# Kernel optimization log

Measured on AMD Instinct MI355X. Metric: run time of the kernel, lower is better.

## Reference

```python
import jax, jax.numpy as jnp
import numpy as np

B, T, C, H = 4, 2048, 2048, 16
D = C // H  # head dim = 128


def setup_inputs() -> dict:
    key = jax.random.key(0)
    k1, k2, k3, k4 = jax.random.split(key, 4)
    x = jax.random.normal(k1, (B, T, C), dtype=jnp.float32)
    # per-token key mask; force token 0 valid so no causal row is fully masked
    tok_mask = jax.random.randint(k2, (B, T), 0, 2).astype(bool).at[:, 0].set(True)
    s = 1.0 / np.sqrt(C).astype(np.float32)
    W_qkv = jax.random.normal(k3, (C, 3 * C), dtype=jnp.float32) * s
    W_proj = jax.random.normal(k4, (C, C), dtype=jnp.float32) * s
    return {"x": x, "tok_mask": tok_mask, "W_qkv": W_qkv, "W_proj": W_proj}


def reference(x, tok_mask, W_qkv, W_proj):
    Bx, Tx, Cx = x.shape
    qkv = x @ W_qkv                              # [B,T,3C]
    q, k, v = jnp.split(qkv, 3, axis=-1)
    q = q.reshape(Bx, Tx, H, D)
    k = k.reshape(Bx, Tx, H, D)
    v = v.reshape(Bx, Tx, H, D)
    scale = 1.0 / np.sqrt(D).astype(np.float32)
    scores = jnp.einsum('bqhd,bkhd->bhqk', q, k) * scale  # [B,H,T,T]
    causal = jnp.tril(jnp.ones((Tx, Tx), dtype=bool))      # [T,T]
    # tok_mask broadcasts over the query dim (key mask), AND-ed with causal
    mask = tok_mask[:, None, :] & causal                   # [B,T,T]
    scores = jnp.where(mask[:, None, :, :], scores, -jnp.inf)
    attn = jax.nn.softmax(scores, axis=-1)                 # dropout p=0 -> identity
    y = jnp.einsum('bhqk,bkhd->bqhd', attn, v).reshape(Bx, Tx, Cx)
    return y @ W_proj
```

## Files before the change

### kernel.cpp

```cpp
#include <hip/hip_runtime.h>
#include <hip/hip_bf16.h>
#include <stdint.h>

typedef __bf16 bf16;
typedef __bf16 bf16x8 __attribute__((ext_vector_type(8)));
typedef float f32x4 __attribute__((ext_vector_type(4)));
typedef unsigned short u16;
typedef unsigned int u32;

constexpr int NB = 4;
constexpr int NT = 2048;
constexpr int NC = 2048;
constexpr int NH = 16;
constexpr int ND = 128;
constexpr int NC3 = 6144;

__device__ __forceinline__ void gload16(const void* g, void* l) {
  __builtin_amdgcn_global_load_lds((const __attribute__((address_space(1))) void*)g,
                                   (__attribute__((address_space(3))) void*)l, 16, 0, 0);
}

__device__ __forceinline__ u32 pack_bf16(float a, float b) {
  return (u32)__builtin_bit_cast(u16, (bf16)a) | ((u32)__builtin_bit_cast(u16, (bf16)b) << 16);
}

__global__ __launch_bounds__(256) void ingest_k(const float* __restrict__ raw, bf16* __restrict__ out, long n) {
  long i = ((long)blockIdx.x * 256 + threadIdx.x) * 8;
  if (i >= n) return;
  f32x4 a = *(const f32x4*)(raw + i), b = *(const f32x4*)(raw + i + 4);
  bf16x8 o;
  o[0] = (bf16)a[0]; o[1] = (bf16)a[1]; o[2] = (bf16)a[2]; o[3] = (bf16)a[3];
  o[4] = (bf16)b[0]; o[5] = (bf16)b[1]; o[6] = (bf16)b[2]; o[7] = (bf16)b[3];
  *(bf16x8*)(out + i) = o;
}

__global__ void mask_prep_k(const void* raw, char* out) {
  __shared__ int s_gt1, s_oddnz, s_allb, s_allf, s_allh;
  if (threadIdx.x == 0) { s_gt1 = 0; s_oddnz = 0; s_allb = 1; s_allf = 1; s_allh = 1; }
  __syncthreads();
  const unsigned int* mw = (const unsigned int*)raw;
  int gt1 = 0, oddnz = 0, allb = 1, allf = 1, allh = 1;
  for (int i = threadIdx.x; i < 2048; i += 256) {
    unsigned v = mw[i];
    if (v > 1u) gt1 = 1;
    if ((i & 1) && v) oddnz = 1;
#pragma unroll
    for (int bb = 0; bb < 4; ++bb) { unsigned by = (v >> (8*bb)) & 0xffu; if (by > 1u) allb = 0; }
    if (v != 0u && v != 0x3F800000u) allf = 0;
    unsigned lo = v & 0xffffu, hi = v >> 16;
    if ((lo != 0u && lo != 0x3F80u) || (hi != 0u && hi != 0x3F80u)) allh = 0;
  }
  if (gt1) atomicOr(&s_gt1, 1);
  if (oddnz) atomicOr(&s_oddnz, 1);
  if (!allb) atomicAnd(&s_allb, 0);
  if (!allf) atomicAnd(&s_allf, 0);
  if (!allh) atomicAnd(&s_allh, 0);
  __syncthreads();
  int mode;
  if (!s_gt1)       mode = s_oddnz ? 0 : 2;
  else if (s_allf)  mode = 3;
  else if (s_allb)  mode = 1;
  else if (s_allh)  mode = 4;
  else              mode = 0;
  for (int i = threadIdx.x; i < NB*NT; i += 256) {
    int v;
    if (mode == 0)      v = (((const int*)raw)[i] != 0);
    else if (mode == 1) v = (((const unsigned char*)raw)[i] != 0);
    else if (mode == 2) v = (((const long long*)raw)[i] != 0);
    else if (mode == 3) v = (((const unsigned int*)raw)[i] != 0);
    else                v = (((const unsigned short*)raw)[i] != 0);
    out[i] = (char)v;
  }
}

__global__ __launch_bounds__(256) void transpose_f32_k(const float* __restrict__ in, bf16* __restrict__ out,
                                                       int in_rs, int out_rs) {
  __shared__ __align__(16) bf16 t[64][72];
  const int r0 = blockIdx.y << 6, c0 = blockIdx.x << 6;
  const int tid = threadIdx.x;
#pragma unroll
  for (int i = 0; i < 4; ++i) {
    int slot = i*256 + tid, row = slot >> 4, c4 = slot & 15;
    f32x4 v = *(const f32x4*)(in + (long)(r0 + row)*in_rs + c0 + c4*4);
#pragma unroll
    for (int e = 0; e < 4; ++e) t[c4*4 + e][row] = (bf16)v[e];
  }
  __syncthreads();
#pragma unroll
  for (int i = 0; i < 2; ++i) {
    int slot = i*256 + tid, row = slot >> 3, c8 = slot & 7;
    bf16x8 v = *(const bf16x8*)(&t[row][c8*8]);
    *(bf16x8*)(out + (long)(c0 + row)*out_rs + r0 + c8*8) = v;
  }
}

__global__ __launch_bounds__(256) void vtrans_k(const bf16* __restrict__ qkv, bf16* __restrict__ vt) {
  __shared__ __align__(16) bf16 t[64][72];
  const int tt = blockIdx.x, dh = blockIdx.y, bh = blockIdx.z;
  const int b = bh >> 4, h = bh & 15;
  const int tid = threadIdx.x;
  const bf16* src = qkv + (long)(b*NT + tt*64)*NC3 + (2*NC + h*ND + dh*64);
#pragma unroll
  for (int i = 0; i < 2; ++i) {
    int slot = i*256 + tid, row = slot >> 3, c8 = slot & 7;
    bf16x8 v = *(const bf16x8*)(src + (long)row*NC3 + c8*8);
#pragma unroll
    for (int e = 0; e < 8; ++e) t[c8*8 + e][row] = v[e];
  }
  __syncthreads();
  bf16* dst = vt + ((long)bh*ND + dh*64)*NT + tt*64;
#pragma unroll
  for (int i = 0; i < 2; ++i) {
    int slot = i*256 + tid, row = slot >> 3, c8 = slot & 7;
    bf16x8 v = *(const bf16x8*)(&t[row][c8*8]);
    *(bf16x8*)(dst + (long)row*NT + c8*8) = v;
  }
}

#define G256_READ_A(qm_) \
  _Pragma("unroll") \
  for (int mi = 0; mi < 4; ++mi) { \
    _Pragma("unroll") \
    for (int kk = 0; kk < 2; ++kk) { \
      const int ri = (qm_)*64 + mi*16 + r; \
      af[mi*2+kk] = *(const bf16x8*)(Ac + wm*16384 + ri*128 + (((kk*4 + g) ^ (ri & 7)) << 4)); \
    } \
  }
#define G256_READ_B(qn_) \
  _Pragma("unroll") \
  for (int ni = 0; ni < 2; ++ni) { \
    _Pragma("unroll") \
    for (int kk = 0; kk < 2; ++kk) { \
      const int ri = (qn_)*32 + ni*16 + r; \
      bfr[ni*2+kk] = *(const bf16x8*)(Bc + wn*8192 + ri*128 + (((kk*4 + g) ^ (ri & 7)) << 4)); \
    } \
  }
#define G256_MFMA(mb_, nb_) \
  __builtin_amdgcn_s_setprio(1); \
  _Pragma("unroll") \
  for (int mi = 0; mi < 4; ++mi) \
    _Pragma("unroll") \
    for (int ni = 0; ni < 2; ++ni) \
      _Pragma("unroll") \
      for (int kk = 0; kk < 2; ++kk) \
        acc[(mb_)+mi][(nb_)+ni] = __builtin_amdgcn_mfma_f32_16x16x32_bf16(af[mi*2+kk], bfr[ni*2+kk], acc[(mb_)+mi][(nb_)+ni], 0, 0, 0); \
  __builtin_amdgcn_s_setprio(0);
#define G256_EDGE(vm_) \
  asm volatile("s_waitcnt vmcnt(" #vm_ ")" ::: "memory"); \
  __builtin_amdgcn_s_barrier(); \
  __builtin_amdgcn_sched_barrier(0);
#define G256_EDGE_NOVM() \
  asm volatile("" ::: "memory"); \
  __builtin_amdgcn_s_barrier(); \
  __builtin_amdgcn_sched_barrier(0);

template <typename OT>
__global__ __launch_bounds__(512, 2) void gemm256_k(const bf16* __restrict__ A, const bf16* __restrict__ BT,
                                                    OT* __restrict__ Cout, int M, int N, int K, int nbx) {
  const int nwg = gridDim.x;
  const int bid = blockIdx.x;
  const int cpx = nwg >> 3;
  const int swz = (bid & 7) * cpx + (bid >> 3);
  const int bx = swz % nbx, by = swz / nbx;
  const long m0 = (long)by << 8, n0 = (long)bx << 8;

  const int tid = threadIdx.x, w = tid >> 6, l = tid & 63, g = l >> 4, r = l & 15;
  const int wm = w >> 2, wn = w & 3;

  __shared__ __align__(16) char As[2][32768];
  __shared__ __align__(16) char Bs[2][32768];

  long aoff2[4], boff2[4];
  int alds[4], blds[4];
#pragma unroll
  for (int i = 0; i < 4; ++i) {
    int s = i*256 + (tid & 255);
    int ri = s >> 3, c = s & 7, cp = c ^ (ri & 7);
    aoff2[i] = (m0 + wm*128 + ri) * (long)K + cp*8;
    alds[i] = wm*16384 + ((i*256 + (w & 3)*64) << 4);
    int s2 = i*128 + wm*64 + l;
    int ri2 = s2 >> 3, c2 = s2 & 7, cp2 = c2 ^ (ri2 & 7);
    boff2[i] = (n0 + wn*64 + ri2) * (long)K + cp2*8;
    blds[i] = wn*8192 + ((i*128 + wm*64) << 4);
  }

  const f32x4 z4 = {0.f, 0.f, 0.f, 0.f};
  f32x4 acc[8][4];
#pragma unroll
  for (int i = 0; i < 8; ++i)
#pragma unroll
    for (int j = 0; j < 4; ++j) acc[i][j] = z4;

  const int nk = K >> 6;
  gload16(A + aoff2[0], As[0] + alds[0]);
  gload16(A + aoff2[1], As[0] + alds[1]);
  gload16(BT + boff2[0], Bs[0] + blds[0]);
  gload16(BT + boff2[1], Bs[0] + blds[1]);
  gload16(A + aoff2[2], As[0] + alds[2]);
  gload16(A + aoff2[3], As[0] + alds[3]);
  gload16(BT + boff2[2], Bs[0] + blds[2]);
  gload16(BT + boff2[3], Bs[0] + blds[3]);
  G256_EDGE(4);

  bf16x8 af[8], bfr[4];

  for (int t = 0; t < nk - 1; ++t) {
    const int cur = t & 1;
    const char* Ac = As[cur];
    const char* Bc = Bs[cur];
    char* An = As[cur ^ 1];
    char* Bn = Bs[cur ^ 1];
    const long ko = (long)(t + 1) << 6;

    G256_READ_A(0); G256_READ_B(0);
    gload16(A + aoff2[0] + ko, An + alds[0]);
    gload16(A + aoff2[1] + ko, An + alds[1]);
    gload16(BT + boff2[0] + ko, Bn + blds[0]);
    gload16(BT + boff2[1] + ko, Bn + blds[1]);
    G256_MFMA(0, 0);
    G256_EDGE(6);

    G256_READ_A(1);
    gload16(A + aoff2[2] + ko, An + alds[2]);
    gload16(A + aoff2[3] + ko, An + alds[3]);
    gload16(BT + boff2[2] + ko, Bn + blds[2]);
    gload16(BT + boff2[3] + ko, Bn + blds[3]);
    G256_MFMA(4, 0);
    G256_EDGE(8);

    G256_READ_B(1);
    G256_MFMA(4, 2);
    G256_EDGE_NOVM();

    G256_READ_A(0);
    G256_MFMA(0, 2);
    G256_EDGE(4);
  }

  {
    const int cur = (nk - 1) & 1;
    const char* Ac = As[cur];
    const char* Bc = Bs[cur];
    G256_READ_A(0); G256_READ_B(0);
    G256_MFMA(0, 0);
    G256_EDGE(2);
    G256_READ_A(1);
    G256_MFMA(4, 0);
    G256_EDGE(0);
    G256_READ_B(1);
    G256_MFMA(4, 2);
    G256_EDGE_NOVM();
    G256_READ_A(0);
    G256_MFMA(0, 2);
  }

#pragma unroll
  for (int mi = 0; mi < 8; ++mi)
#pragma unroll
    for (int ni = 0; ni < 4; ++ni)
#pragma unroll
      for (int j = 0; j < 4; ++j) {
        long mr = m0 + wm*128 + mi*16 + 4*g + j;
        long nc = n0 + wn*64 + ni*16 + r;
        Cout[mr*(long)N + nc] = (OT)acc[mi][ni][j];
      }
}

__global__ __launch_bounds__(256, 2) void attn_k(const bf16* __restrict__ qkv, const bf16* __restrict__ vt,
                                                 const char* __restrict__ maskC, bf16* __restrict__ y) {
  const int qx = blockIdx.x, h = blockIdx.y, b = blockIdx.z;
  const int qb = (qx & 1) ? (15 - (qx >> 1)) : (qx >> 1);
  const int tid = threadIdx.x, w = tid >> 6, l = tid & 63, g = l >> 4, r = l & 15;
  const int q0 = qb << 7;
  const int bh = b*NH + h;
  const int ntiles = (qb << 1) + 2;
  const int qrowA = q0 + w*32 + r;
  const int qrowB = qrowA + 16;

  __shared__ __align__(16) char Klds[2][16384];
  __shared__ __align__(16) char Vlds[2][16384];
  __shared__ __align__(16) char Plds[16384];
  char* PlA = Plds + (w << 12);
  char* PlB = PlA + 2048;

  const char* mc = maskC + b*NT;

  long koff[4], voff[4];
  int klo[4];
#pragma unroll
  for (int i = 0; i < 4; ++i) {
    int slot = i*256 + tid;
    int row = slot >> 4, c = slot & 15, cp = c ^ (row & 7);
    koff[i] = (long)row*NC3 + cp*8;
    klo[i] = (i*256 + w*64) << 4;
    int vrow = slot >> 3, vc = slot & 7, vcp = vc ^ (vrow & 7);
    voff[i] = (long)vrow*NT + vcp*8;
  }
  const bf16* kbase0 = qkv + (long)(b*NT)*NC3 + (NC + h*ND);
  const bf16* vbase0 = vt + (long)bh*ND*NT;

  bf16x8 qfA[4], qfB[4];
  {
    const bf16* qpA = qkv + (long)(b*NT + qrowA)*NC3 + h*ND + g*8;
    const bf16* qpB = qkv + (long)(b*NT + qrowB)*NC3 + h*ND + g*8;
#pragma unroll
    for (int dk = 0; dk < 4; ++dk) {
      qfA[dk] = *(const bf16x8*)(qpA + dk*32);
      qfB[dk] = *(const bf16x8*)(qpB + dk*32);
    }
  }

  const f32x4 z4 = {0.f, 0.f, 0.f, 0.f};
  f32x4 accA[8], accB[8];
#pragma unroll
  for (int i = 0; i < 8; ++i) { accA[i] = z4; accB[i] = z4; }
  float m_runA = 0.0f, l_runA = 0.0f;
  float m_runB = 0.0f, l_runB = 0.0f;

  const float SCL = 0.08838834764831845f * 1.4426950408889634f;

#pragma unroll
  for (int i = 0; i < 4; ++i) {
    gload16(kbase0 + koff[i], Klds[0] + klo[i]);
    gload16(vbase0 + voff[i], Vlds[0] + klo[i]);
  }
  __syncthreads();

  for (int kt = 0; kt < ntiles; ++kt) {
    const int cur = kt & 1;
    if (kt + 1 < ntiles) {
      const bf16* kb = kbase0 + (long)((kt+1)*64)*NC3;
      const bf16* vb = vbase0 + (kt+1)*64;
#pragma unroll
      for (int i = 0; i < 4; ++i) {
        gload16(kb + koff[i], Klds[cur^1] + klo[i]);
        gload16(vb + voff[i], Vlds[cur^1] + klo[i]);
      }
    }
    const char* Kl = Klds[cur];
    const char* Vl = Vlds[cur];
    const int key0 = kt*64;
    const bool actB = (key0 <= q0 + w*32 + 31);
    const bool actA = (key0 <= q0 + w*32 + 15);

    if (actB) {
      u32 mw_[4];
#pragma unroll
      for (int kc = 0; kc < 4; ++kc) mw_[kc] = *(const u32*)(mc + key0 + kc*16 + 4*g);

      float tvA[4][4], tvB[4][4];
      __builtin_amdgcn_s_setprio(1);
#pragma unroll
      for (int kc = 0; kc < 4; ++kc) {
        const int krow = kc*16 + r;
        bf16x8 kf[4];
#pragma unroll
        for (int dk = 0; dk < 4; ++dk)
          kf[dk] = *(const bf16x8*)(Kl + krow*256 + (((dk*4 + g) ^ (krow & 7)) << 4));
        f32x4 sB = z4;
#pragma unroll
        for (int dk = 0; dk < 4; ++dk)
          sB = __builtin_amdgcn_mfma_f32_16x16x32_bf16(kf[dk], qfB[dk], sB, 0, 0, 0);
        f32x4 sA = z4;
        if (actA) {
#pragma unroll
          for (int dk = 0; dk < 4; ++dk)
            sA = __builtin_amdgcn_mfma_f32_16x16x32_bf16(kf[dk], qfA[dk], sA, 0, 0, 0);
        }
#pragma unroll
        for (int j = 0; j < 4; ++j) {
          const int key = key0 + kc*16 + 4*g + j;
          const bool km = ((mw_[kc] >> (8*j)) & 0xffu) != 0;
          tvB[kc][j] = (km && key <= qrowB) ? sB[j]*SCL : -3.0e38f;
          tvA[kc][j] = (km && key <= qrowA) ? sA[j]*SCL : -3.0e38f;
        }
      }
      __builtin_amdgcn_s_setprio(0);

      {
        float tmax = -3.0e38f;
#pragma unroll
        for (int kc = 0; kc < 4; ++kc)
#pragma unroll
          for (int j = 0; j < 4; ++j) tmax = fmaxf(tmax, tvB[kc][j]);
        tmax = fmaxf(tmax, __shfl_xor(tmax, 16));
        tmax = fmaxf(tmax, __shfl_xor(tmax, 32));
        if (!__all(tmax <= m_runB + 8.0f)) {
          float mn = fmaxf(m_runB, tmax);
          float al = exp2f(m_runB - mn);
          m_runB = mn;
          l_runB *= al;
          float alj[4];
#pragma unroll
          for (int j = 0; j < 4; ++j) alj[j] = __shfl(al, 4*g + j);
#pragma unroll
          for (int d0 = 0; d0 < 8; ++d0)
#pragma unroll
            for (int j = 0; j < 4; ++j) accB[d0][j] *= alj[j];
        }
        float rs = 0.f;
#pragma unroll
        for (int kc = 0; kc < 4; ++kc) {
          float p0 = exp2f(tvB[kc][0] - m_runB), p1 = exp2f(tvB[kc][1] - m_runB);
          float p2 = exp2f(tvB[kc][2] - m_runB), p3 = exp2f(tvB[kc][3] - m_runB);
          rs += (p0 + p1) + (p2 + p3);
          const int off = (kc*32 + g*8) ^ ((r & 7) << 4);
          uint2 wv; wv.x = pack_bf16(p0, p1); wv.y = pack_bf16(p2, p3);
          *(uint2*)(PlB + r*128 + off) = wv;
        }
        rs += __shfl_xor(rs, 16);
        rs += __shfl_xor(rs, 32);
        l_runB += rs;
      }
      if (actA) {
        float tmax = -3.0e38f;
#pragma unroll
        for (int kc = 0; kc < 4; ++kc)
#pragma unroll
          for (int j = 0; j < 4; ++j) tmax = fmaxf(tmax, tvA[kc][j]);
        tmax = fmaxf(tmax, __shfl_xor(tmax, 16));
        tmax = fmaxf(tmax, __shfl_xor(tmax, 32));
        if (!__all(tmax <= m_runA + 8.0f)) {
          float mn = fmaxf(m_runA, tmax);
          float al = exp2f(m_runA - mn);
          m_runA = mn;
          l_runA *= al;
          float alj[4];
#pragma unroll
          for (int j = 0; j < 4; ++j) alj[j] = __shfl(al, 4*g + j);
#pragma unroll
          for (int d0 = 0; d0 < 8; ++d0)
#pragma unroll
            for (int j = 0; j < 4; ++j) accA[d0][j] *= alj[j];
        }
        float rs = 0.f;
#pragma unroll
        for (int kc = 0; kc < 4; ++kc) {
          float p0 = exp2f(tvA[kc][0] - m_runA), p1 = exp2f(tvA[kc][1] - m_runA);
          float p2 = exp2f(tvA[kc][2] - m_runA), p3 = exp2f(tvA[kc][3] - m_runA);
          rs += (p0 + p1) + (p2 + p3);
          const int off = (kc*32 + g*8) ^ ((r & 7) << 4);
          uint2 wv; wv.x = pack_bf16(p0, p1); wv.y = pack_bf16(p2, p3);
          *(uint2*)(PlA + r*128 + off) = wv;
        }
        rs += __shfl_xor(rs, 16);
        rs += __shfl_xor(rs, 32);
        l_runA += rs;
      }

      asm volatile("s_waitcnt lgkmcnt(0)" ::: "memory");
      __builtin_amdgcn_sched_barrier(0);
      bf16x8 paA[2], paB[2];
#pragma unroll
      for (int kk = 0; kk < 2; ++kk) {
        paB[kk] = *(const bf16x8*)(PlB + r*128 + ((kk*64 + g*16) ^ ((r & 7) << 4)));
        paA[kk] = *(const bf16x8*)(PlA + r*128 + ((kk*64 + g*16) ^ ((r & 7) << 4)));
      }

      __builtin_amdgcn_s_setprio(1);
#pragma unroll
      for (int d0 = 0; d0 < 8; ++d0) {
        const int vrow = d0*16 + r;
#pragma unroll
        for (int kk = 0; kk < 2; ++kk) {
          bf16x8 vf = *(const bf16x8*)(Vl + vrow*128 + (((kk*4 + g) ^ (vrow & 7)) << 4));
          accB[d0] = __builtin_amdgcn_mfma_f32_16x16x32_bf16(paB[kk], vf, accB[d0], 0, 0, 0);
          if (actA) accA[d0] = __builtin_amdgcn_mfma_f32_16x16x32_bf16(paA[kk], vf, accA[d0], 0, 0, 0);
        }
      }
      __builtin_amdgcn_s_setprio(0);
    }
    __syncthreads();
  }

  {
    float lrA[4], lrB[4];
#pragma unroll
    for (int j = 0; j < 4; ++j) {
      lrA[j] = __shfl(l_runA, 4*g + j);
      lrB[j] = __shfl(l_runB, 4*g + j);
    }
#pragma unroll
    for (int d0 = 0; d0 < 8; ++d0)
#pragma unroll
      for (int j = 0; j < 4; ++j) {
        int qrA = q0 + w*32 + 4*g + j;
        y[(long)(b*NT + qrA)*NC + h*ND + d0*16 + r] = (bf16)(accA[d0][j] / lrA[j]);
        y[(long)(b*NT + qrA + 16)*NC + h*ND + d0*16 + r] = (bf16)(accB[d0][j] / lrB[j]);
      }
  }
}

extern "C" void kernel_launch(void* const* d_in, const int* in_sizes, int n_in,
                              void* d_out, int out_size, void* d_ws, size_t ws_size,
                              hipStream_t stream) {
  const float* xr     = (const float*)d_in[0];
  const void*  tok    = d_in[1];
  const float* wqkvr  = (const float*)d_in[2];
  const float* wprojr = (const float*)d_in[3];
  float* out = (float*)d_out;
  char* ws = (char*)d_ws;

  bf16* qkv    = (bf16*)(ws);
  bf16* yattn  = (bf16*)(ws + 100663296L);
  bf16* wT     = (bf16*)(ws + 134217728L);
  bf16* wpT    = (bf16*)(ws + 159383552L);
  bf16* xb     = (bf16*)(ws + 167772160L);
  bf16* vtb    = xb;
  char* maskC  = (char*)(ws + 201326592L);

  mask_prep_k<<<1, 256, 0, stream>>>(tok, maskC);
  ingest_k<<<8192, 256, 0, stream>>>(xr, xb, 16777216L);
  transpose_f32_k<<<dim3(96, 32), 256, 0, stream>>>(wqkvr, wT, NC3, NC);
  transpose_f32_k<<<dim3(32, 32), 256, 0, stream>>>(wprojr, wpT, NC, NC);
  gemm256_k<bf16><<<768, 512, 0, stream>>>(xb, wT, qkv, 8192, 6144, 2048, 24);
  vtrans_k<<<dim3(32, 2, 64), 256, 0, stream>>>(qkv, vtb);
  attn_k<<<dim3(16, 16, 4), 256, 0, stream>>>(qkv, vtb, maskC, yattn);
  gemm256_k<float><<<256, 512, 0, stream>>>(yattn, wpT, out, 8192, 2048, 2048, 8);
}
```

Measured before the change: 547.6 us.

## Shrink attention key tiles to 32 with triple-buffered prefetch and LDS mask

Halves the key tile to 32 keys and moves from double to triple buffering, so loads are issued two tiles ahead. The per-tile __syncthreads is replaced by a counted vmcnt wait plus a barrier. The per-batch key mask is staged into LDS once per block, and V/P layouts use a new 4-way swizzle. The aim is to hide load latency behind compute and cut LDS use per block, at the price of twice as many iterations and barriers plus more softmax-rescale overhead per key.

```diff
diff --git a/kernel.cpp b/kernel.cpp
--- a/kernel.cpp
+++ b/kernel.cpp
@@ -14,6 +14,8 @@
 constexpr int NH = 16;
 constexpr int ND = 128;
 constexpr int NC3 = 6144;
+
+#define VSWZ(x) ((((x) & 3)) ^ ((((x) >> 2) & 3)))
 
 __device__ __forceinline__ void gload16(const void* g, void* l) {
   __builtin_amdgcn_global_load_lds((const __attribute__((address_space(1))) void*)g,
@@ -273,28 +275,29 @@
   const int tid = threadIdx.x, w = tid >> 6, l = tid & 63, g = l >> 4, r = l & 15;
   const int q0 = qb << 7;
   const int bh = b*NH + h;
-  const int ntiles = (qb << 1) + 2;
+  const int ntiles = (qb << 2) + 4;
   const int qrowA = q0 + w*32 + r;
   const int qrowB = qrowA + 16;
 
-  __shared__ __align__(16) char Klds[2][16384];
-  __shared__ __align__(16) char Vlds[2][16384];
-  __shared__ __align__(16) char Plds[16384];
-  char* PlA = Plds + (w << 12);
-  char* PlB = PlA + 2048;
-
-  const char* mc = maskC + b*NT;
-
-  long koff[4], voff[4];
-  int klo[4];
-#pragma unroll
-  for (int i = 0; i < 4; ++i) {
+  __shared__ __align__(16) char Klds[3][8192];
+  __shared__ __align__(16) char Vlds[3][8192];
+  __shared__ __align__(16) char Plds[8192];
+  __shared__ char Mc[2048];
+  char* PlA = Plds + (w << 11);
+  char* PlB = PlA + 1024;
+
+  for (int i = tid; i < q0 + 128; i += 256) Mc[i] = maskC[b*NT + i];
+
+  long koff[2], voff[2];
+  int slo[2];
+#pragma unroll
+  for (int i = 0; i < 2; ++i) {
     int slot = i*256 + tid;
     int row = slot >> 4, c = slot & 15, cp = c ^ (row & 7);
     koff[i] = (long)row*NC3 + cp*8;
-    klo[i] = (i*256 + w*64) << 4;
-    int vrow = slot >> 3, vc = slot & 7, vcp = vc ^ (vrow & 7);
+    int vrow = slot >> 2, vc = slot & 3, vcp = vc ^ VSWZ(vrow);
     voff[i] = (long)vrow*NT + vcp*8;
+    slo[i] = (i*256 + w*64) << 4;
   }
   const bf16* kbase0 = qkv + (long)(b*NT)*NC3 + (NC + h*ND);
   const bf16* vbase0 = vt + (long)bh*ND*NT;
@@ -319,39 +322,54 @@
 
   const float SCL = 0.08838834764831845f * 1.4426950408889634f;
 
-#pragma unroll
-  for (int i = 0; i < 4; ++i) {
-    gload16(kbase0 + koff[i], Klds[0] + klo[i]);
-    gload16(vbase0 + voff[i], Vlds[0] + klo[i]);
-  }
   __syncthreads();
 
+#pragma unroll
+  for (int i = 0; i < 2; ++i) {
+    gload16(kbase0 + koff[i], Klds[0] + slo[i]);
+    gload16(vbase0 + voff[i], Vlds[0] + slo[i]);
+  }
+  {
+    const bf16* kb = kbase0 + 32L*NC3;
+    const bf16* vb = vbase0 + 32;
+#pragma unroll
+    for (int i = 0; i < 2; ++i) {
+      gload16(kb + koff[i], Klds[1] + slo[i]);
+      gload16(vb + voff[i], Vlds[1] + slo[i]);
+    }
+  }
+  asm volatile("s_waitcnt vmcnt(4)" ::: "memory");
+  __builtin_amdgcn_s_barrier();
+  __builtin_amdgcn_sched_barrier(0);
+
+  int cur = 0;
   for (int kt = 0; kt < ntiles; ++kt) {
-    const int cur = kt & 1;
-    if (kt + 1 < ntiles) {
-      const bf16* kb = kbase0 + (long)((kt+1)*64)*NC3;
-      const bf16* vb = vbase0 + (kt+1)*64;
-#pragma unroll
-      for (int i = 0; i < 4; ++i) {
-        gload16(kb + koff[i], Klds[cur^1] + klo[i]);
-        gload16(vb + voff[i], Vlds[cur^1] + klo[i]);
+    const int key0 = kt << 5;
+    const bool stg = (kt + 2 < ntiles);
+    if (stg) {
+      const int bufS = (cur >= 1) ? cur - 1 : cur + 2;
+      const bf16* kb = kbase0 + (long)((kt + 2) * 32) * NC3;
+      const bf16* vb = vbase0 + (kt + 2) * 32;
+#pragma unroll
+      for (int i = 0; i < 2; ++i) {
+        gload16(kb + koff[i], Klds[bufS] + slo[i]);
+        gload16(vb + voff[i], Vlds[bufS] + slo[i]);
       }
     }
     const char* Kl = Klds[cur];
     const char* Vl = Vlds[cur];
-    const int key0 = kt*64;
     const bool actB = (key0 <= q0 + w*32 + 31);
     const bool actA = (key0 <= q0 + w*32 + 15);
 
     if (actB) {
-      u32 mw_[4];
-#pragma unroll
-      for (int kc = 0; kc < 4; ++kc) mw_[kc] = *(const u32*)(mc + key0 + kc*16 + 4*g);
-
-      float tvA[4][4], tvB[4][4];
+      u32 mw_[2];
+#pragma unroll
+      for (int kc = 0; kc < 2; ++kc) mw_[kc] = *(const u32*)(Mc + key0 + kc*16 + 4*g);
+
+      float tvA[2][4], tvB[2][4];
       __builtin_amdgcn_s_setprio(1);
 #pragma unroll
-      for (int kc = 0; kc < 4; ++kc) {
+      for (int kc = 0; kc < 2; ++kc) {
         const int krow = kc*16 + r;
         bf16x8 kf[4];
 #pragma unroll
@@ -380,7 +398,7 @@
       {
         float tmax = -3.0e38f;
 #pragma unroll
-        for (int kc = 0; kc < 4; ++kc)
+        for (int kc = 0; kc < 2; ++kc)
 #pragma unroll
           for (int j = 0; j < 4; ++j) tmax = fmaxf(tmax, tvB[kc][j]);
         tmax = fmaxf(tmax, __shfl_xor(tmax, 16));
@@ -400,13 +418,13 @@
         }
         float rs = 0.f;
 #pragma unroll
-        for (int kc = 0; kc < 4; ++kc) {
+        for (int kc = 0; kc < 2; ++kc) {
           float p0 = exp2f(tvB[kc][0] - m_runB), p1 = exp2f(tvB[kc][1] - m_runB);
           float p2 = exp2f(tvB[kc][2] - m_runB), p3 = exp2f(tvB[kc][3] - m_runB);
           rs += (p0 + p1) + (p2 + p3);
-          const int off = (kc*32 + g*8) ^ ((r & 7) << 4);
+          const int off = (((kc*2 + (g >> 1)) ^ VSWZ(r)) << 4) + (g & 1)*8;
           uint2 wv; wv.x = pack_bf16(p0, p1); wv.y = pack_bf16(p2, p3);
-          *(uint2*)(PlB + r*128 + off) = wv;
+          *(uint2*)(PlB + r*64 + off) = wv;
         }
         rs += __shfl_xor(rs, 16);
         rs += __shfl_xor(rs, 32);
@@ -415,7 +433,7 @@
       if (actA) {
         float tmax = -3.0e38f;
 #pragma unroll
-        for (int kc = 0; kc < 4; ++kc)
+        for (int kc = 0; kc < 2; ++kc)
 #pragma unroll
           for (int j = 0; j < 4; ++j) tmax = fmaxf(tmax, tvA[kc][j]);
         tmax = fmaxf(tmax, __shfl_xor(tmax, 16));
@@ -435,13 +453,13 @@
         }
         float rs = 0.f;
 #pragma unroll
-        for (int kc = 0; kc < 4; ++kc) {
+        for (int kc = 0; kc < 2; ++kc) {
           float p0 = exp2f(tvA[kc][0] - m_runA), p1 = exp2f(tvA[kc][1] - m_runA);
           float p2 = exp2f(tvA[kc][2] - m_runA), p3 = exp2f(tvA[kc][3] - m_runA);
           rs += (p0 + p1) + (p2 + p3);
-          const int off = (kc*32 + g*8) ^ ((r & 7) << 4);
+          const int off = (((kc*2 + (g >> 1)) ^ VSWZ(r)) << 4) + (g & 1)*8;
           uint2 wv; wv.x = pack_bf16(p0, p1); wv.y = pack_bf16(p2, p3);
-          *(uint2*)(PlA + r*128 + off) = wv;
+          *(uint2*)(PlA + r*64 + off) = wv;
         }
         rs += __shfl_xor(rs, 16);
         rs += __shfl_xor(rs, 32);
@@ -450,27 +468,28 @@
 
       asm volatile("s_waitcnt lgkmcnt(0)" ::: "memory");
       __builtin_amdgcn_sched_barrier(0);
-      bf16x8 paA[2], paB[2];
-#pragma unroll
-      for (int kk = 0; kk < 2; ++kk) {
-        paB[kk] = *(const bf16x8*)(PlB + r*128 + ((kk*64 + g*16) ^ ((r & 7) << 4)));
-        paA[kk] = *(const bf16x8*)(PlA + r*128 + ((kk*64 + g*16) ^ ((r & 7) << 4)));
-      }
+      bf16x8 paA, paB;
+      paB = *(const bf16x8*)(PlB + r*64 + ((g ^ VSWZ(r)) << 4));
+      paA = *(const bf16x8*)(PlA + r*64 + ((g ^ VSWZ(r)) << 4));
 
       __builtin_amdgcn_s_setprio(1);
 #pragma unroll
       for (int d0 = 0; d0 < 8; ++d0) {
         const int vrow = d0*16 + r;
-#pragma unroll
-        for (int kk = 0; kk < 2; ++kk) {
-          bf16x8 vf = *(const bf16x8*)(Vl + vrow*128 + (((kk*4 + g) ^ (vrow & 7)) << 4));
-          accB[d0] = __builtin_amdgcn_mfma_f32_16x16x32_bf16(paB[kk], vf, accB[d0], 0, 0, 0);
-          if (actA) accA[d0] = __builtin_amdgcn_mfma_f32_16x16x32_bf16(paA[kk], vf, accA[d0], 0, 0, 0);
-        }
+        bf16x8 vf = *(const bf16x8*)(Vl + vrow*64 + ((g ^ VSWZ(vrow)) << 4));
+        accB[d0] = __builtin_amdgcn_mfma_f32_16x16x32_bf16(paB, vf, accB[d0], 0, 0, 0);
+        if (actA) accA[d0] = __builtin_amdgcn_mfma_f32_16x16x32_bf16(paA, vf, accA[d0], 0, 0, 0);
       }
       __builtin_amdgcn_s_setprio(0);
     }
-    __syncthreads();
+
+    if (kt + 1 < ntiles) {
+      if (stg) { asm volatile("s_waitcnt vmcnt(4)" ::: "memory"); }
+      else     { asm volatile("s_waitcnt vmcnt(0)" ::: "memory"); }
+      __builtin_amdgcn_s_barrier();
+      __builtin_amdgcn_sched_barrier(0);
+    }
+    cur = (cur == 2) ? 0 : cur + 1;
   }
 
   {
```

Measured after the change: 590.5 us. +7.8%, slower.
